# Performance work log

Hardware: AMD Instinct MI355X
Metric: run time of the kernel (lower is better)

The kernel has to match this reference:

```python
import jax, jax.numpy as jnp
from jax import lax
import numpy as np

B, T, I, H = 64, 2048, 256, 512


def setup_inputs() -> dict:
    key = jax.random.key(0)
    ks = jax.random.split(key, 5)
    stdv = 1.0 / np.sqrt(H)
    return {
        "x": jax.random.normal(ks[0], (B, T, I), dtype=jnp.float32),
        "w_ih0": jax.random.normal(ks[1], (H, I), dtype=jnp.float32) * 0.01,
        "w_hh0": jax.random.uniform(ks[2], (H,), dtype=jnp.float32, minval=-stdv, maxval=stdv),
        "b_ih0": jnp.zeros((H,), dtype=jnp.float32),
        "w_ih1": jax.random.normal(ks[3], (H, H), dtype=jnp.float32) * 0.01,
        "w_hh1": jax.random.uniform(ks[4], (H,), dtype=jnp.float32, minval=-stdv, maxval=stdv),
        "b_ih1": jnp.zeros((H,), dtype=jnp.float32),
    }


def _indrnn_layer(inp, w_ih, w_hh, b_ih):
    # Precompute input projection for all timesteps in one GEMM
    # (identical math to per-step F.linear). pre: (B, T, H)
    pre = jnp.einsum("bti,hi->bth", inp, w_ih) + b_ih
    h0 = jnp.zeros((inp.shape[0], w_hh.shape[0]), dtype=inp.dtype)

    def step(h, p_t):  # p_t: (B, H)
        h = jax.nn.relu(p_t + w_hh * h)
        return h, h

    _, ys = lax.scan(step, h0, jnp.swapaxes(pre, 0, 1))  # ys: (T, B, H)
    return jnp.swapaxes(ys, 0, 1)  # (B, T, H)


def reference(x, w_ih0, w_hh0, b_ih0, w_ih1, w_hh1, b_ih1):
    out = _indrnn_layer(x, w_ih0, w_hh0, b_ih0)
    out = _indrnn_layer(out, w_ih1, w_hh1, b_ih1)
    return out  # torch module returns (out, None); out.squeeze(2) is a no-op for H>1
```

## Files before the change

kernel.cpp:

```cpp
#include <hip/hip_runtime.h>
#include <hip/hip_bf16.h>


#define BB 64
#define TT 2048
#define II 256
#define HH 512
#define MM (BB * TT)

typedef __attribute__((ext_vector_type(8))) short bf16x8;
typedef __attribute__((ext_vector_type(4))) float f32x4;

__device__ inline unsigned short bf16_rne(float f) {
  unsigned u = __builtin_bit_cast(unsigned, f);
  u += 0x7FFFu + ((u >> 16) & 1u);
  return (unsigned short)(u >> 16);
}
__device__ inline float bf16_val(unsigned short h) {
  unsigned u = ((unsigned)h) << 16;
  return __builtin_bit_cast(float, u);
}

typedef __attribute__((address_space(1))) const void GASV;
typedef __attribute__((address_space(3))) void LASV;
__device__ inline void gload_lds4(const float* g, float* l) {
  __builtin_amdgcn_global_load_lds((GASV*)g, (LASV*)l, 4, 0, 0);
}

template <int K, int MODE>
__global__ __launch_bounds__(256) void gemm_mfma(
    const float* __restrict__ Af, const unsigned short* __restrict__ Ahg,
    const unsigned short* __restrict__ Alg, const float* __restrict__ Wf,
    const unsigned short* __restrict__ Whg, const unsigned short* __restrict__ Wlg,
    const float* __restrict__ bias, float* __restrict__ C) {
  constexpr int BM = 128, BN = 128, BK = 32;
  constexpr int LDT = 40;
  __shared__ unsigned short Ah[BM * LDT], Al[BM * LDT];
  __shared__ unsigned short Bh[BN * LDT], Bl[BN * LDT];

  const int bid = blockIdx.x;
  const int xcd = bid & 7;
  const int local = bid >> 3;
  const int mb = xcd * (MM / BM / 8) + (local >> 2);
  const int nb = local & 3;
  const int m0 = mb * BM, n0 = nb * BN;

  const int tid = threadIdx.x;
  const int lane = tid & 63;
  const int wave = tid >> 6;
  const int wr = wave >> 1, wc = wave & 1;
  const int lrow = lane & 15, lkg = lane >> 4;

  f32x4 acc[4][4] = {};

  const int srow = tid >> 1;
  const int skq = (tid & 1) * 4;
  const int skq8 = (tid & 1) * 16;

  for (int kt = 0; kt < K; kt += BK) {
    float4 av[4], wv[4];
    bf16x8 a8[4], w8[4];
    if constexpr (MODE == 2) {
      const size_t ro = (size_t)(m0 + srow) * K + kt + skq8;
      a8[0] = *(const bf16x8*)(Ahg + ro);
      a8[1] = *(const bf16x8*)(Ahg + ro + 8);
      a8[2] = *(const bf16x8*)(Alg + ro);
      a8[3] = *(const bf16x8*)(Alg + ro + 8);
    } else {
      const float4* Aq = (const float4*)(Af + (size_t)(m0 + srow) * K + kt) + skq;
#pragma unroll
      for (int s = 0; s < 4; ++s) av[s] = Aq[s];
    }
    if constexpr (MODE >= 1) {
      const size_t ro = (size_t)(n0 + srow) * K + kt + skq8;
      w8[0] = *(const bf16x8*)(Whg + ro);
      w8[1] = *(const bf16x8*)(Whg + ro + 8);
      w8[2] = *(const bf16x8*)(Wlg + ro);
      w8[3] = *(const bf16x8*)(Wlg + ro + 8);
    } else {
      const float4* Wq = (const float4*)(Wf + (size_t)(n0 + srow) * K + kt) + skq;
#pragma unroll
      for (int s = 0; s < 4; ++s) wv[s] = Wq[s];
    }

    __syncthreads();

    if constexpr (MODE == 2) {
      *(bf16x8*)&Ah[srow * LDT + skq8] = a8[0];
      *(bf16x8*)&Ah[srow * LDT + skq8 + 8] = a8[1];
      *(bf16x8*)&Al[srow * LDT + skq8] = a8[2];
      *(bf16x8*)&Al[srow * LDT + skq8 + 8] = a8[3];
    } else {
#pragma unroll
      for (int s = 0; s < 4; ++s) {
        const int kk = (skq + s) * 4;
        const float fa[4] = {av[s].x, av[s].y, av[s].z, av[s].w};
        ushort4 ah4, al4;
        unsigned short* pah = (unsigned short*)&ah4;
        unsigned short* pal = (unsigned short*)&al4;
#pragma unroll
        for (int e = 0; e < 4; ++e) {
          const unsigned short h1 = bf16_rne(fa[e]);
          pah[e] = h1;
          pal[e] = bf16_rne(fa[e] - bf16_val(h1));
        }
        *(ushort4*)&Ah[srow * LDT + kk] = ah4;
        *(ushort4*)&Al[srow * LDT + kk] = al4;
      }
    }
    if constexpr (MODE >= 1) {
      *(bf16x8*)&Bh[srow * LDT + skq8] = w8[0];
      *(bf16x8*)&Bh[srow * LDT + skq8 + 8] = w8[1];
      *(bf16x8*)&Bl[srow * LDT + skq8] = w8[2];
      *(bf16x8*)&Bl[srow * LDT + skq8 + 8] = w8[3];
    } else {
#pragma unroll
      for (int s = 0; s < 4; ++s) {
        const int kk = (skq + s) * 4;
        const float fw[4] = {wv[s].x, wv[s].y, wv[s].z, wv[s].w};
        ushort4 wh4, wl4;
        unsigned short* pwh = (unsigned short*)&wh4;
        unsigned short* pwl = (unsigned short*)&wl4;
#pragma unroll
        for (int e = 0; e < 4; ++e) {
          const unsigned short h2 = bf16_rne(fw[e]);
          pwh[e] = h2;
          pwl[e] = bf16_rne(fw[e] - bf16_val(h2));
        }
        *(ushort4*)&Bh[srow * LDT + kk] = wh4;
        *(ushort4*)&Bl[srow * LDT + kk] = wl4;
      }
    }
    __syncthreads();

    bf16x8 afh[4], afl[4], bfh[4], bfl[4];
#pragma unroll
    for (int i = 0; i < 4; ++i) {
      const int ar = wr * 64 + i * 16 + lrow;
      afh[i] = *(const bf16x8*)&Ah[ar * LDT + lkg * 8];
      afl[i] = *(const bf16x8*)&Al[ar * LDT + lkg * 8];
      const int br = wc * 64 + i * 16 + lrow;
      bfh[i] = *(const bf16x8*)&Bh[br * LDT + lkg * 8];
      bfl[i] = *(const bf16x8*)&Bl[br * LDT + lkg * 8];
    }
#pragma unroll
    for (int i = 0; i < 4; ++i)
#pragma unroll
      for (int j = 0; j < 4; ++j) {
        acc[i][j] = __builtin_amdgcn_mfma_f32_16x16x32_bf16(afh[i], bfh[j], acc[i][j], 0, 0, 0);
        acc[i][j] = __builtin_amdgcn_mfma_f32_16x16x32_bf16(afh[i], bfl[j], acc[i][j], 0, 0, 0);
        acc[i][j] = __builtin_amdgcn_mfma_f32_16x16x32_bf16(afl[i], bfh[j], acc[i][j], 0, 0, 0);
      }
  }

  const int rb = (lane >> 4) * 4;
#pragma unroll
  for (int j = 0; j < 4; ++j) {
    const int col = n0 + wc * 64 + j * 16 + lrow;
    const float bv = bias[col];
#pragma unroll
    for (int i = 0; i < 4; ++i) {
      const int row0 = m0 + wr * 64 + i * 16 + rb;
#pragma unroll
      for (int r = 0; r < 4; ++r)
        C[(size_t)(row0 + r) * HH + col] = acc[i][j][r] + bv;
    }
  }
}

template <bool SPLIT>
__global__ __launch_bounds__(64) void indrnn_scan2(
    const float* __restrict__ pre, const float* __restrict__ w_hh,
    float* __restrict__ outf, unsigned short* __restrict__ outh,
    unsigned short* __restrict__ outl) {
  constexpr int CH = 16, NCH = TT / CH, AHEAD = 3;
  __shared__ float lds[4 * CH * 64];
  const int lane = threadIdx.x;
  const int gid = blockIdx.x * 64 + lane;
  const int h = gid & (HH - 1);
  const size_t colbase = (size_t)(gid >> 9) * TT * HH + h;

  const float w = w_hh[h];
  float hv = 0.f;

  auto issue = [&](int c) {
    const float* g = pre + colbase + (size_t)(c * CH) * HH;
    float* l = &lds[(c & 3) * CH * 64];
#pragma unroll
    for (int tt = 0; tt < CH; ++tt) gload_lds4(g + (size_t)tt * HH, l + tt * 64);
  };

  issue(0);
  issue(1);
  issue(2);
  for (int c = 0; c < NCH; ++c) {
    if (c + AHEAD < NCH) issue(c + AHEAD);
    asm volatile("s_waitcnt vmcnt(48)" ::: "memory");
    __builtin_amdgcn_sched_barrier(0);
    const float* l = &lds[(c & 3) * CH * 64];
#pragma unroll
    for (int tt = 0; tt < CH; ++tt) {
      const float p = l[tt * 64 + lane];
      hv = fmaxf(fmaf(w, hv, p), 0.f);
      const size_t gi = colbase + (size_t)(c * CH + tt) * HH;
      if constexpr (SPLIT) {
        const unsigned short hh = bf16_rne(hv);
        outh[gi] = hh;
        outl[gi] = bf16_rne(hv - bf16_val(hh));
      } else {
        outf[gi] = hv;
      }
    }
  }
}

__global__ __launch_bounds__(256) void convert_w(const float* __restrict__ W,
                                                 unsigned short* __restrict__ Wh,
                                                 unsigned short* __restrict__ Wl,
                                                 int n) {
  const int i = blockIdx.x * 256 + threadIdx.x;
  if (i < n) {
    const float f = W[i];
    const unsigned short hh = bf16_rne(f);
    Wh[i] = hh;
    Wl[i] = bf16_rne(f - bf16_val(hh));
  }
}

extern "C" void kernel_launch(void* const* d_in, const int* in_sizes, int n_in,
                              void* d_out, int out_size, void* d_ws, size_t ws_size,
                              hipStream_t stream) {
  const float* x     = (const float*)d_in[0];
  const float* w_ih0 = (const float*)d_in[1];
  const float* w_hh0 = (const float*)d_in[2];
  const float* b_ih0 = (const float*)d_in[3];
  const float* w_ih1 = (const float*)d_in[4];
  const float* w_hh1 = (const float*)d_in[5];
  const float* b_ih1 = (const float*)d_in[6];
  float* out = (float*)d_out;
  float* pre0 = (float*)d_ws;
  char* wsb = (char*)d_ws;

  const size_t OFF_A1H = 268435456ull;
  const size_t OFF_A1L = OFF_A1H + 134217728ull;
  const size_t OFF_W0H = OFF_A1L + 134217728ull;
  const size_t OFF_W0L = OFF_W0H + 262144ull;
  const size_t OFF_W1H = OFF_W0L + 262144ull;
  const size_t OFF_W1L = OFF_W1H + 524288ull;
  const size_t NEED = OFF_W1L + 524288ull;

  const int ntiles = (MM / 128) * (HH / 128);

  if (ws_size >= NEED) {
    unsigned short* A1h = (unsigned short*)(wsb + OFF_A1H);
    unsigned short* A1l = (unsigned short*)(wsb + OFF_A1L);
    unsigned short* W0h = (unsigned short*)(wsb + OFF_W0H);
    unsigned short* W0l = (unsigned short*)(wsb + OFF_W0L);
    unsigned short* W1h = (unsigned short*)(wsb + OFF_W1H);
    unsigned short* W1l = (unsigned short*)(wsb + OFF_W1L);

    convert_w<<<(HH * II) / 256, 256, 0, stream>>>(w_ih0, W0h, W0l, HH * II);
    convert_w<<<(HH * HH) / 256, 256, 0, stream>>>(w_ih1, W1h, W1l, HH * HH);
    gemm_mfma<II, 1><<<ntiles, 256, 0, stream>>>(x, nullptr, nullptr, nullptr, W0h, W0l, b_ih0, pre0);
    indrnn_scan2<true><<<(BB * HH) / 64, 64, 0, stream>>>(pre0, w_hh0, nullptr, A1h, A1l);
    gemm_mfma<HH, 2><<<ntiles, 256, 0, stream>>>(nullptr, A1h, A1l, nullptr, W1h, W1l, b_ih1, out);
    indrnn_scan2<false><<<(BB * HH) / 64, 64, 0, stream>>>(out, w_hh1, out, nullptr, nullptr);
  } else {
    gemm_mfma<II, 0><<<ntiles, 256, 0, stream>>>(x, nullptr, nullptr, w_ih0, nullptr, nullptr, b_ih0, pre0);
    indrnn_scan2<false><<<(BB * HH) / 64, 64, 0, stream>>>(pre0, w_hh0, pre0, nullptr, nullptr);
    gemm_mfma<HH, 0><<<ntiles, 256, 0, stream>>>(pre0, nullptr, nullptr, w_ih1, nullptr, nullptr, b_ih1, out);
    indrnn_scan2<false><<<(BB * HH) / 64, 64, 0, stream>>>(out, w_hh1, out, nullptr, nullptr);
  }
}
```

Before: 944.4 us.

## Use time-contiguous tiled layout between GEMMs and scans, packing hi/lo bf16

The GEMM epilogue now writes pre-activations in a [b][h/64][t][64] tiled layout, so each scan block reads contiguous 16-byte chunks per timestep group instead of 4-byte loads strided by H. The layer-1 scan packs its hi/lo bf16 split into a single 32-bit word in the same tiled layout, and the second GEMM unpacks it on load. This is meant to cut memory-transaction overhead in the scan kernels. The cost is scattered 4-byte stores in the GEMM epilogue and some unpack work in the second GEMM's load stage.

```diff
diff --git a/kernel.cpp b/kernel.cpp
--- a/kernel.cpp
+++ b/kernel.cpp
@@ -9,6 +9,7 @@
 #define MM (BB * TT)
 
 typedef __attribute__((ext_vector_type(8))) short bf16x8;
+typedef __attribute__((ext_vector_type(8))) unsigned short u16x8;
 typedef __attribute__((ext_vector_type(4))) float f32x4;
 
 __device__ inline unsigned short bf16_rne(float f) {
@@ -26,13 +27,16 @@
 __device__ inline void gload_lds4(const float* g, float* l) {
   __builtin_amdgcn_global_load_lds((GASV*)g, (LASV*)l, 4, 0, 0);
 }
-
-template <int K, int MODE>
+__device__ inline void gload_lds16(const float* g, float* l) {
+  __builtin_amdgcn_global_load_lds((GASV*)g, (LASV*)l, 16, 0, 0);
+}
+
+template <int K, int MODE, bool OUTTILED>
 __global__ __launch_bounds__(256) void gemm_mfma(
-    const float* __restrict__ Af, const unsigned short* __restrict__ Ahg,
-    const unsigned short* __restrict__ Alg, const float* __restrict__ Wf,
-    const unsigned short* __restrict__ Whg, const unsigned short* __restrict__ Wlg,
-    const float* __restrict__ bias, float* __restrict__ C) {
+    const float* __restrict__ Af, const unsigned* __restrict__ Apg,
+    const float* __restrict__ Wf, const unsigned short* __restrict__ Whg,
+    const unsigned short* __restrict__ Wlg, const float* __restrict__ bias,
+    float* __restrict__ C) {
   constexpr int BM = 128, BN = 128, BK = 32;
   constexpr int LDT = 40;
   __shared__ unsigned short Ah[BM * LDT], Al[BM * LDT];
@@ -59,13 +63,16 @@
 
   for (int kt = 0; kt < K; kt += BK) {
     float4 av[4], wv[4];
-    bf16x8 a8[4], w8[4];
-    if constexpr (MODE == 2) {
-      const size_t ro = (size_t)(m0 + srow) * K + kt + skq8;
-      a8[0] = *(const bf16x8*)(Ahg + ro);
-      a8[1] = *(const bf16x8*)(Ahg + ro + 8);
-      a8[2] = *(const bf16x8*)(Alg + ro);
-      a8[3] = *(const bf16x8*)(Alg + ro + 8);
+    bf16x8 w8[4];
+    uint4 q[4];
+    if constexpr (MODE == 3) {
+      const int m = m0 + srow;
+      const int b = m >> 11, t = m & 2047;
+      const int kk = kt + skq8;
+      const unsigned* ap =
+          Apg + ((size_t)(b * 8 + (kk >> 6)) * TT + t) * 64 + (kk & 63);
+#pragma unroll
+      for (int s = 0; s < 4; ++s) q[s] = *(const uint4*)(ap + s * 4);
     } else {
       const float4* Aq = (const float4*)(Af + (size_t)(m0 + srow) * K + kt) + skq;
 #pragma unroll
@@ -85,11 +92,22 @@
 
     __syncthreads();
 
-    if constexpr (MODE == 2) {
-      *(bf16x8*)&Ah[srow * LDT + skq8] = a8[0];
-      *(bf16x8*)&Ah[srow * LDT + skq8 + 8] = a8[1];
-      *(bf16x8*)&Al[srow * LDT + skq8] = a8[2];
-      *(bf16x8*)&Al[srow * LDT + skq8 + 8] = a8[3];
+    if constexpr (MODE == 3) {
+      const unsigned qq[16] = {q[0].x, q[0].y, q[0].z, q[0].w, q[1].x, q[1].y,
+                               q[1].z, q[1].w, q[2].x, q[2].y, q[2].z, q[2].w,
+                               q[3].x, q[3].y, q[3].z, q[3].w};
+      u16x8 ha, hb2, la, lb;
+#pragma unroll
+      for (int e = 0; e < 8; ++e) {
+        ha[e] = (unsigned short)(qq[e] >> 16);
+        la[e] = (unsigned short)(qq[e] & 0xFFFFu);
+        hb2[e] = (unsigned short)(qq[e + 8] >> 16);
+        lb[e] = (unsigned short)(qq[e + 8] & 0xFFFFu);
+      }
+      *(u16x8*)&Ah[srow * LDT + skq8] = ha;
+      *(u16x8*)&Ah[srow * LDT + skq8 + 8] = hb2;
+      *(u16x8*)&Al[srow * LDT + skq8] = la;
+      *(u16x8*)&Al[srow * LDT + skq8 + 8] = lb;
     } else {
 #pragma unroll
       for (int s = 0; s < 4; ++s) {
@@ -162,17 +180,76 @@
     for (int i = 0; i < 4; ++i) {
       const int row0 = m0 + wr * 64 + i * 16 + rb;
 #pragma unroll
-      for (int r = 0; r < 4; ++r)
-        C[(size_t)(row0 + r) * HH + col] = acc[i][j][r] + bv;
-    }
-  }
-}
-
-template <bool SPLIT>
-__global__ __launch_bounds__(64) void indrnn_scan2(
+      for (int r = 0; r < 4; ++r) {
+        const float v = acc[i][j][r] + bv;
+        if constexpr (OUTTILED) {
+          const int m = row0 + r;
+          const int b = m >> 11, t = m & 2047;
+          C[((size_t)(b * 8 + (col >> 6)) * TT + t) * 64 + (col & 63)] = v;
+        } else {
+          C[(size_t)(row0 + r) * HH + col] = v;
+        }
+      }
+    }
+  }
+}
+
+template <bool PACK>
+__global__ __launch_bounds__(64) void indrnn_scan_tiled(
+    const float* __restrict__ in, const float* __restrict__ w_hh,
+    float* __restrict__ outf, unsigned* __restrict__ outp) {
+  constexpr int CH = 16, NCH = TT / CH;
+  __shared__ float lds[4 * CH * 64];
+  const int lane = threadIdx.x;
+  const int b = blockIdx.x >> 3, hb = blockIdx.x & 7;
+  const size_t tilebase = (size_t)(b * 8 + hb) * TT * 64;
+
+  const float w = w_hh[hb * 64 + lane];
+  float hv = 0.f;
+
+  auto issue = [&](int c) {
+    const float* cb = in + tilebase + (size_t)c * CH * 64;
+    float* l = &lds[(c & 3) * (CH * 64)];
+#pragma unroll
+    for (int k = 0; k < 4; ++k) {
+      gload_lds16(cb + k * 256 + (lane >> 4) * 64 + (lane & 15) * 4, l + k * 256);
+    }
+  };
+
+  issue(0);
+  issue(1);
+  issue(2);
+  for (int c = 0; c < NCH; ++c) {
+    if (c + 3 < NCH) issue(c + 3);
+    if (c == 0)
+      asm volatile("s_waitcnt vmcnt(12)" ::: "memory");
+    else if (c == 1)
+      asm volatile("s_waitcnt vmcnt(28)" ::: "memory");
+    else if (c == 2 || c >= NCH - 3)
+      asm volatile("s_waitcnt vmcnt(44)" ::: "memory");
+    else
+      asm volatile("s_waitcnt vmcnt(60)" ::: "memory");
+    __builtin_amdgcn_sched_barrier(0);
+    const float* l = &lds[(c & 3) * (CH * 64)];
+#pragma unroll
+    for (int tt = 0; tt < CH; ++tt) {
+      const float p = l[tt * 64 + lane];
+      hv = fmaxf(fmaf(w, hv, p), 0.f);
+      if constexpr (PACK) {
+        const unsigned short hi = bf16_rne(hv);
+        const unsigned short lo = bf16_rne(hv - bf16_val(hi));
+        outp[tilebase + (size_t)(c * CH + tt) * 64 + lane] =
+            ((unsigned)hi << 16) | (unsigned)lo;
+      } else {
+        outf[((size_t)b * TT + c * CH + tt) * HH + hb * 64 + lane] = hv;
+      }
+    }
+  }
+}
+
+__global__ __launch_bounds__(64) void indrnn_scan_strided(
     const float* __restrict__ pre, const float* __restrict__ w_hh,
-    float* __restrict__ outf, unsigned short* __restrict__ outh,
-    unsigned short* __restrict__ outl) {
+    float* __restrict__ outf) {
   constexpr int CH = 16, NCH = TT / CH, AHEAD = 3;
   __shared__ float lds[4 * CH * 64];
   const int lane = threadIdx.x;
@@ -195,21 +272,14 @@
   issue(2);
   for (int c = 0; c < NCH; ++c) {
     if (c + AHEAD < NCH) issue(c + AHEAD);
-    asm volatile("s_waitcnt vmcnt(48)" ::: "memory");
+    asm volatile("s_waitcnt vmcnt(16)" ::: "memory");
     __builtin_amdgcn_sched_barrier(0);
     const float* l = &lds[(c & 3) * CH * 64];
 #pragma unroll
     for (int tt = 0; tt < CH; ++tt) {
       const float p = l[tt * 64 + lane];
       hv = fmaxf(fmaf(w, hv, p), 0.f);
-      const size_t gi = colbase + (size_t)(c * CH + tt) * HH;
-      if constexpr (SPLIT) {
-        const unsigned short hh = bf16_rne(hv);
-        outh[gi] = hh;
-        outl[gi] = bf16_rne(hv - bf16_val(hh));
-      } else {
-        outf[gi] = hv;
-      }
+      outf[colbase + (size_t)(c * CH + tt) * HH] = hv;
     }
   }
 }
@@ -241,9 +311,8 @@
   float* pre0 = (float*)d_ws;
   char* wsb = (char*)d_ws;
 
-  const size_t OFF_A1H = 268435456ull;
-  const size_t OFF_A1L = OFF_A1H + 134217728ull;
-  const size_t OFF_W0H = OFF_A1L + 134217728ull;
+  const size_t OFF_A1P = 268435456ull;
+  const size_t OFF_W0H = OFF_A1P + 268435456ull;
   const size_t OFF_W0L = OFF_W0H + 262144ull;
   const size_t OFF_W1H = OFF_W0L + 262144ull;
   const size_t OFF_W1L = OFF_W1H + 524288ull;
@@ -252,8 +321,7 @@
   const int ntiles = (MM / 128) * (HH / 128);
 
   if (ws_size >= NEED) {
-    unsigned short* A1h = (unsigned short*)(wsb + OFF_A1H);
-    unsigned short* A1l = (unsigned short*)(wsb + OFF_A1L);
+    unsigned* A1p = (unsigned*)(wsb + OFF_A1P);
     unsigned short* W0h = (unsigned short*)(wsb + OFF_W0H);
     unsigned short* W0l = (unsigned short*)(wsb + OFF_W0L);
     unsigned short* W1h = (unsigned short*)(wsb + OFF_W1H);
@@ -261,14 +329,18 @@
 
     convert_w<<<(HH * II) / 256, 256, 0, stream>>>(w_ih0, W0h, W0l, HH * II);
     convert_w<<<(HH * HH) / 256, 256, 0, stream>>>(w_ih1, W1h, W1l, HH * HH);
-    gemm_mfma<II, 1><<<ntiles, 256, 0, stream>>>(x, nullptr, nullptr, nullptr, W0h, W0l, b_ih0, pre0);
-    indrnn_scan2<true><<<(BB * HH) / 64, 64, 0, stream>>>(pre0, w_hh0, nullptr, A1h, A1l);
-    gemm_mfma<HH, 2><<<ntiles, 256, 0, stream>>>(nullptr, A1h, A1l, nullptr, W1h, W1l, b_ih1, out);
-    indrnn_scan2<false><<<(BB * HH) / 64, 64, 0, stream>>>(out, w_hh1, out, nullptr, nullptr);
+    gemm_mfma<II, 1, true><<<ntiles, 256, 0, stream>>>(
+        x, nullptr, nullptr, W0h, W0l, b_ih0, pre0);
+    indrnn_scan_tiled<true><<<BB * 8, 64, 0, stream>>>(pre0, w_hh0, nullptr, A1p);
+    gemm_mfma<HH, 3, true><<<ntiles, 256, 0, stream>>>(
+        nullptr, A1p, nullptr, W1h, W1l, b_ih1, pre0);
+    indrnn_scan_tiled<false><<<BB * 8, 64, 0, stream>>>(pre0, w_hh1, out, nullptr);
   } else {
-    gemm_mfma<II, 0><<<ntiles, 256, 0, stream>>>(x, nullptr, nullptr, w_ih0, nullptr, nullptr, b_ih0, pre0);
-    indrnn_scan2<false><<<(BB * HH) / 64, 64, 0, stream>>>(pre0, w_hh0, pre0, nullptr, nullptr);
-    gemm_mfma<HH, 0><<<ntiles, 256, 0, stream>>>(pre0, nullptr, nullptr, w_ih1, nullptr, nullptr, b_ih1, out);
-    indrnn_scan2<false><<<(BB * HH) / 64, 64, 0, stream>>>(out, w_hh1, out, nullptr, nullptr);
-  }
-}
+    gemm_mfma<II, 0, false><<<ntiles, 256, 0, stream>>>(
+        x, nullptr, w_ih0, nullptr, nullptr, b_ih0, pre0);
+    indrnn_scan_strided<<<(BB * HH) / 64, 64, 0, stream>>>(pre0, w_hh0, pre0);
+    gemm_mfma<HH, 0, false><<<ntiles, 256, 0, stream>>>(
+        pre0, nullptr, w_ih1, nullptr, nullptr, b_ih1, out);
+    indrnn_scan_strided<<<(BB * HH) / 64, 64, 0, stream>>>(out, w_hh1, out);
+  }
+}
```

Result: no change. 953.9 us (+1.0%).
